# Kernel tuning notes

Measured on AMD Instinct MI355X. Metric: run time of the kernel, lower is better.

## Reference

```python
import jax, jax.numpy as jnp
import numpy as np

D_MODEL = 2048
N_Q_HEADS = 32
N_KV_HEADS = 8
D_HEAD = 64
D_MLP = 8192
NORM_EPS = 1e-5
INIT_RANGE = 0.02
IGNORE = -100000.0
B, S = 2, 2048


def setup_inputs() -> dict:
    key = jax.random.key(0)
    ks = jax.random.split(key, 8)
    return {
        "resid_pre": jax.random.normal(ks[0], (B, S, D_MODEL), dtype=jnp.float32),
        "W_Q": jax.random.normal(ks[1], (N_Q_HEADS, D_MODEL, D_HEAD), dtype=jnp.float32) * INIT_RANGE,
        "W_K": jax.random.normal(ks[2], (N_KV_HEADS, D_MODEL, D_HEAD), dtype=jnp.float32) * INIT_RANGE,
        "W_V": jax.random.normal(ks[3], (N_KV_HEADS, D_MODEL, D_HEAD), dtype=jnp.float32) * INIT_RANGE,
        "W_O": jax.random.normal(ks[4], (N_KV_HEADS, D_HEAD, D_MODEL), dtype=jnp.float32) * INIT_RANGE,
        "g1": jnp.ones((D_MODEL,), jnp.float32),
        "b1": jnp.zeros((D_MODEL,), jnp.float32),
        "g2": jnp.ones((D_MODEL,), jnp.float32),
        "b2": jnp.zeros((D_MODEL,), jnp.float32),
        "W_in": jax.random.normal(ks[5], (D_MODEL, D_MLP), dtype=jnp.float32) * INIT_RANGE,
        "b_in": jnp.zeros((D_MLP,), jnp.float32),
        "W_out": jax.random.normal(ks[6], (D_MLP, D_MODEL), dtype=jnp.float32) * INIT_RANGE,
        "b_out": jnp.zeros((D_MODEL,), jnp.float32),
    }


def rmsnorm(x, g, b):
    # torch.var (unbiased=False) is mean-centered variance, but x itself is
    # divided (not centered) -- faithful to the source.
    mu = jnp.mean(x, axis=-1, keepdims=True)
    var = jnp.mean(jnp.square(x - mu), axis=-1, keepdims=True)
    std = jnp.sqrt(var + NORM_EPS)
    return (x / std) * g + b


def attention(x, W_Q, W_K, W_V, W_O):
    b, s, _ = x.shape
    q = jnp.einsum('bpd,hde->bphe', x, W_Q)            # [b, s, n_q, d_head]
    k = jnp.einsum('bpd,hde->bphe', x, W_K)            # [b, s, n_kv, d_head]
    v = jnp.einsum('bpd,hde->bphe', x, W_V)            # [b, s, n_kv, d_head]
    g_size = N_Q_HEADS // N_KV_HEADS
    # rearrange '(n_kv g) d' with n_kv outer, group inner
    q = q.reshape(b, s, N_KV_HEADS, g_size, D_HEAD)
    # source einsum sums over the group dim (g not in output) -- faithful
    scores = jnp.einsum('bqkgd,bskd->bkqs', q, k) / jnp.sqrt(jnp.float32(D_HEAD))
    mask = jnp.triu(jnp.ones((s, s), dtype=bool), k=1)
    scores = jnp.where(mask, jnp.float32(IGNORE), scores)
    pattern = jax.nn.softmax(scores, axis=-1)          # [b, n_kv, q, s]
    z = jnp.einsum('bskd,bkqs->bqkd', v, pattern)      # [b, q, n_kv, d_head]
    return jnp.einsum('bqkd,kde->bqe', z, W_O)


def ffn(x, W_in, b_in, W_out, b_out):
    pre = jnp.einsum('bpd,dm->bpm', x, W_in) + b_in
    post = jax.nn.relu(pre)
    return jnp.einsum('bpm,md->bpd', post, W_out) + b_out


def reference(resid_pre, W_Q, W_K, W_V, W_O, g1, b1, g2, b2, W_in, b_in, W_out, b_out):
    resid_mid = attention(rmsnorm(resid_pre, g1, b1), W_Q, W_K, W_V, W_O) + resid_pre
    resid_post = ffn(rmsnorm(resid_mid, g2, b2), W_in, b_in, W_out, b_out) + resid_mid
    return resid_post
```

## Files before the change

### kernel.cpp

```cpp
#include <hip/hip_runtime.h>
#include <hip/hip_bf16.h>


using bf16 = __hip_bfloat16;
typedef __bf16 bf16x8_t __attribute__((ext_vector_type(8)));
typedef float  f32x4_t  __attribute__((ext_vector_type(4)));

#define D_MODEL 2048
#define SEQ     2048
#define NB      2
#define NTOK    4096
#define NKV     8
#define DHEAD   64
#define DMLP    8192
#define NQKV    1536

__device__ inline void storev(float* p, float v) { *p = v; }
__device__ inline void storev(bf16* p, float v)  { *p = __float2bfloat16(v); }

__device__ inline __bf16 tobf(float x) {
    union { __hip_bfloat16 h; __bf16 b; } u;
    u.h = __float2bfloat16(x);
    return u.b;
}

__global__ __launch_bounds__(256) void transpose_f32_bf16_kernel(
    const float* __restrict__ in, bf16* __restrict__ out, int K, int N)
{
    __shared__ float tile[32][33];
    const int n0 = blockIdx.x * 32, k0 = blockIdx.y * 32;
    const int tx = threadIdx.x & 31, ty = threadIdx.x >> 5;
    #pragma unroll
    for (int i = 0; i < 32; i += 8)
        tile[ty + i][tx] = in[(size_t)(k0 + ty + i) * N + n0 + tx];
    __syncthreads();
    #pragma unroll
    for (int i = 0; i < 32; i += 8)
        out[(size_t)(n0 + ty + i) * K + k0 + tx] = __float2bfloat16(tile[tx][ty + i]);
}

__global__ __launch_bounds__(256) void head_transpose_kernel(
    const float* __restrict__ in, bf16* __restrict__ out, int ngroup)
{
    __shared__ float tile[32][65];
    const int kv = blockIdx.y;
    const int k0 = blockIdx.x * 32;
    const int t  = threadIdx.x;
    const int e  = t & 63, kk = t >> 6;
    #pragma unroll
    for (int i = 0; i < 32; i += 4) {
        float s = 0.f;
        for (int g = 0; g < ngroup; ++g)
            s += in[((size_t)(kv * ngroup + g) * 2048 + k0 + kk + i) * 64 + e];
        tile[kk + i][e] = s;
    }
    __syncthreads();
    const int k = t & 31, ee = t >> 5;
    #pragma unroll
    for (int i = 0; i < 64; i += 8)
        out[(size_t)(kv * 64 + ee + i) * 2048 + k0 + k] = __float2bfloat16(tile[k][ee + i]);
}

__global__ __launch_bounds__(256) void rmsnorm_kernel(
    const float* __restrict__ x, const float* __restrict__ g,
    const float* __restrict__ b, bf16* __restrict__ out)
{
    const int row = blockIdx.x;
    const int t = threadIdx.x;
    const float* xr = x + (size_t)row * D_MODEL;
    float4 a0 = *reinterpret_cast<const float4*>(xr + t * 8);
    float4 a1 = *reinterpret_cast<const float4*>(xr + t * 8 + 4);
    float v[8] = {a0.x, a0.y, a0.z, a0.w, a1.x, a1.y, a1.z, a1.w};
    float sum = 0.f, sumsq = 0.f;
    #pragma unroll
    for (int j = 0; j < 8; ++j) { sum += v[j]; sumsq += v[j] * v[j]; }
    #pragma unroll
    for (int o = 1; o < 64; o <<= 1) {
        sum   += __shfl_xor(sum, o);
        sumsq += __shfl_xor(sumsq, o);
    }
    __shared__ float rs[4], rq[4];
    if ((t & 63) == 0) { rs[t >> 6] = sum; rq[t >> 6] = sumsq; }
    __syncthreads();
    sum   = rs[0] + rs[1] + rs[2] + rs[3];
    sumsq = rq[0] + rq[1] + rq[2] + rq[3];
    const float mu  = sum * (1.f / D_MODEL);
    const float var = sumsq * (1.f / D_MODEL) - mu * mu;
    const float rstd = 1.f / sqrtf(var + 1e-5f);
    const int c = t * 8;
    float4 g0 = *reinterpret_cast<const float4*>(g + c);
    float4 g1 = *reinterpret_cast<const float4*>(g + c + 4);
    float4 b0 = *reinterpret_cast<const float4*>(b + c);
    float4 b1 = *reinterpret_cast<const float4*>(b + c + 4);
    float gg[8] = {g0.x, g0.y, g0.z, g0.w, g1.x, g1.y, g1.z, g1.w};
    float bb[8] = {b0.x, b0.y, b0.z, b0.w, b1.x, b1.y, b1.z, b1.w};
    bf16* op = out + (size_t)row * D_MODEL + c;
    #pragma unroll
    for (int j = 0; j < 8; ++j) op[j] = __float2bfloat16(v[j] * rstd * gg[j] + bb[j]);
}

template<int BM, typename TC, bool BIAS, bool RELU, bool RESID>
__global__ __launch_bounds__(512, 2) void gemm_pipe_kernel(
    const bf16* __restrict__ A, const bf16* __restrict__ Bt,
    TC* __restrict__ C, const float* __restrict__ bias,
    const float* __restrict__ resid, int M, int N, int K, int nbx)
{
    constexpr int BN   = 256;
    constexpr int BK   = 64;
    constexpr int MREP = BM / 32;
    constexpr int AI   = (BM * BK) / 4096;

    __shared__ __align__(16) bf16 As[2][BM * BK];
    __shared__ __align__(16) bf16 Bs[2][BN * BK];

    const int nwg = gridDim.x;
    const int swz = (blockIdx.x & 7) * (nwg >> 3) + (blockIdx.x >> 3);
    const int nby = nwg / nbx;
    const int by  = swz % nby;
    const int bx  = swz / nby;
    const int row0 = by * BM, col0 = bx * BN;

    const int t  = threadIdx.x;
    const int w  = t >> 6, ln = t & 63;
    const int wm = w >> 2, wn = w & 3;
    const int lr = ln & 15, hi = ln >> 4;

    const int srow = w * 8 + (ln >> 3);
    const int skx  = ((ln & 7) ^ (ln >> 3)) * 8;

    f32x4_t acc[MREP][4];
    #pragma unroll
    for (int m = 0; m < MREP; ++m)
        #pragma unroll
        for (int n = 0; n < 4; ++n) acc[m][n] = (f32x4_t){0.f, 0.f, 0.f, 0.f};

    const int NT = K / BK;

    {
        const bf16* ga = A  + (size_t)(row0 + srow) * K + skx;
        const bf16* gb = Bt + (size_t)(col0 + srow) * K + skx;
        #pragma unroll
        for (int i = 0; i < AI; ++i)
            __builtin_amdgcn_global_load_lds(
                (const __attribute__((address_space(1))) void*)(ga + (size_t)i * 64 * K),
                (__attribute__((address_space(3))) void*)(&As[0][i * 4096 + w * 512]), 16, 0, 0);
        #pragma unroll
        for (int i = 0; i < 4; ++i)
            __builtin_amdgcn_global_load_lds(
                (const __attribute__((address_space(1))) void*)(gb + (size_t)i * 64 * K),
                (__attribute__((address_space(3))) void*)(&Bs[0][i * 4096 + w * 512]), 16, 0, 0);
    }

    for (int tt = 0; tt < NT; ++tt) {
        const int c = tt & 1;
        asm volatile("s_waitcnt lgkmcnt(0)" ::: "memory");
        __builtin_amdgcn_sched_barrier(0);
        __builtin_amdgcn_s_barrier();
        __builtin_amdgcn_sched_barrier(0);
        if (tt + 1 < NT) {
            const int d = c ^ 1;
            const int kt = (tt + 1) * BK;
            const bf16* ga = A  + (size_t)(row0 + srow) * K + kt + skx;
            const bf16* gb = Bt + (size_t)(col0 + srow) * K + kt + skx;
            #pragma unroll
            for (int i = 0; i < AI; ++i)
                __builtin_amdgcn_global_load_lds(
                    (const __attribute__((address_space(1))) void*)(ga + (size_t)i * 64 * K),
                    (__attribute__((address_space(3))) void*)(&As[d][i * 4096 + w * 512]), 16, 0, 0);
            #pragma unroll
            for (int i = 0; i < 4; ++i)
                __builtin_amdgcn_global_load_lds(
                    (const __attribute__((address_space(1))) void*)(gb + (size_t)i * 64 * K),
                    (__attribute__((address_space(3))) void*)(&Bs[d][i * 4096 + w * 512]), 16, 0, 0);
            __builtin_amdgcn_sched_barrier(0);
            if constexpr (AI == 4) asm volatile("s_waitcnt vmcnt(8)" ::: "memory");
            else                   asm volatile("s_waitcnt vmcnt(6)" ::: "memory");
        } else {
            asm volatile("s_waitcnt vmcnt(0)" ::: "memory");
        }
        __builtin_amdgcn_sched_barrier(0);
        __builtin_amdgcn_s_barrier();
        __builtin_amdgcn_sched_barrier(0);

        #pragma unroll
        for (int kk = 0; kk < 2; ++kk) {
            bf16x8_t af[MREP], bfr[4];
            #pragma unroll
            for (int m = 0; m < MREP; ++m) {
                const int row = wm * (BM / 2) + m * 16 + lr;
                af[m] = *reinterpret_cast<const bf16x8_t*>(
                    &As[c][row * 64 + ((kk * 32 + hi * 8) ^ ((row & 7) << 3))]);
            }
            #pragma unroll
            for (int n = 0; n < 4; ++n) {
                const int col = wn * 64 + n * 16 + lr;
                bfr[n] = *reinterpret_cast<const bf16x8_t*>(
                    &Bs[c][col * 64 + ((kk * 32 + hi * 8) ^ ((col & 7) << 3))]);
            }
            #pragma unroll
            for (int m = 0; m < MREP; ++m)
                #pragma unroll
                for (int n = 0; n < 4; ++n)
                    acc[m][n] = __builtin_amdgcn_mfma_f32_16x16x32_bf16(af[m], bfr[n], acc[m][n], 0, 0, 0);
        }
    }

    #pragma unroll
    for (int m = 0; m < MREP; ++m) {
        #pragma unroll
        for (int n = 0; n < 4; ++n) {
            const int cgl = col0 + wn * 64 + n * 16 + lr;
            #pragma unroll
            for (int j = 0; j < 4; ++j) {
                const int r = row0 + wm * (BM / 2) + m * 16 + hi * 4 + j;
                float v = acc[m][n][j];
                if constexpr (BIAS)  v += bias[cgl];
                if constexpr (RELU)  v = fmaxf(v, 0.f);
                if constexpr (RESID) v += resid[(size_t)r * N + cgl];
                storev(&C[(size_t)r * N + cgl], v);
            }
        }
    }
}

#define QBLK  128
#define KVBLK 64
#define LP    72

__global__ __launch_bounds__(512) void mfma_attn_kernel(
    const float* __restrict__ qkv, bf16* __restrict__ z)
{
    const int qt = blockIdx.x;
    const int kv = blockIdx.y;
    const int b  = blockIdx.z;
    const int t  = threadIdx.x;
    const int w  = t >> 6;
    const int ln = t & 63;
    const int lr = ln & 15;
    const int hi = ln >> 4;
    const int lk = hi * 8;

    __shared__ __align__(16) bf16 Ks[KVBLK * LP];
    __shared__ __align__(16) bf16 Vt[DHEAD * LP];
    __shared__ __align__(16) bf16 Ps[QBLK * LP];

    bf16x8_t qf[2];
    {
        const int qrow = qt * QBLK + w * 16 + lr;
        const float* qp = qkv + (size_t)(b * SEQ + qrow) * NQKV + kv * 64;
        #pragma unroll
        for (int kk = 0; kk < 2; ++kk) {
            float4 x0 = *reinterpret_cast<const float4*>(qp + kk * 32 + lk);
            float4 x1 = *reinterpret_cast<const float4*>(qp + kk * 32 + lk + 4);
            bf16x8_t v;
            v[0] = tobf(x0.x); v[1] = tobf(x0.y); v[2] = tobf(x0.z); v[3] = tobf(x0.w);
            v[4] = tobf(x1.x); v[5] = tobf(x1.y); v[6] = tobf(x1.z); v[7] = tobf(x1.w);
            qf[kk] = v;
        }
    }

    f32x4_t acc_o[4];
    #pragma unroll
    for (int n = 0; n < 4; ++n) acc_o[n] = (f32x4_t){0.f, 0.f, 0.f, 0.f};
    float m_st[4] = {-1e30f, -1e30f, -1e30f, -1e30f};
    float l_st[4] = {0.f, 0.f, 0.f, 0.f};

    const int qbase_cd = qt * QBLK + w * 16 + hi * 4;

    const int n_tiles = 2 * qt + 2;
    for (int kt = 0; kt < n_tiles; ++kt) {
        const int k0g = kt * KVBLK;
        __syncthreads();
        {
            const int r  = t >> 3;
            const int c8 = (t & 7) * 8;
            const float* kb = qkv + (size_t)(b * SEQ + k0g + r) * NQKV + 512 + kv * 64 + c8;
            float4 k0 = *reinterpret_cast<const float4*>(kb);
            float4 k1 = *reinterpret_cast<const float4*>(kb + 4);
            bf16x8_t kvv;
            kvv[0] = tobf(k0.x); kvv[1] = tobf(k0.y); kvv[2] = tobf(k0.z); kvv[3] = tobf(k0.w);
            kvv[4] = tobf(k1.x); kvv[5] = tobf(k1.y); kvv[6] = tobf(k1.z); kvv[7] = tobf(k1.w);
            *reinterpret_cast<bf16x8_t*>(&Ks[r * LP + c8]) = kvv;
        }
        {
            const int dv = w * 8;
            const float* vb = qkv + (size_t)(b * SEQ + k0g + ln) * NQKV + 1024 + kv * 64 + dv;
            float4 v0 = *reinterpret_cast<const float4*>(vb);
            float4 v1 = *reinterpret_cast<const float4*>(vb + 4);
            float vv[8] = {v0.x, v0.y, v0.z, v0.w, v1.x, v1.y, v1.z, v1.w};
            #pragma unroll
            for (int i = 0; i < 8; ++i)
                Vt[(dv + i) * LP + ln] = __float2bfloat16(vv[i]);
        }
        __syncthreads();

        f32x4_t s[4];
        #pragma unroll
        for (int n = 0; n < 4; ++n) s[n] = (f32x4_t){0.f, 0.f, 0.f, 0.f};
        #pragma unroll
        for (int kk = 0; kk < 2; ++kk) {
            #pragma unroll
            for (int n = 0; n < 4; ++n) {
                bf16x8_t kf = *reinterpret_cast<const bf16x8_t*>(&Ks[(n * 16 + lr) * LP + kk * 32 + lk]);
                s[n] = __builtin_amdgcn_mfma_f32_16x16x32_bf16(qf[kk], kf, s[n], 0, 0, 0);
            }
        }

        const bool need_mask = (kt >= 2 * qt);
        #pragma unroll
        for (int n = 0; n < 4; ++n) {
            const int colg = k0g + n * 16 + lr;
            #pragma unroll
            for (int j = 0; j < 4; ++j) {
                float val = s[n][j] * 0.125f;
                if (need_mask && colg > qbase_cd + j) val = -1e30f;
                s[n][j] = val;
            }
        }

        float alpha[4], mnew[4];
        #pragma unroll
        for (int j = 0; j < 4; ++j) {
            float mx = fmaxf(fmaxf(s[0][j], s[1][j]), fmaxf(s[2][j], s[3][j]));
            mx = fmaxf(mx, __shfl_xor(mx, 1));
            mx = fmaxf(mx, __shfl_xor(mx, 2));
            mx = fmaxf(mx, __shfl_xor(mx, 4));
            mx = fmaxf(mx, __shfl_xor(mx, 8));
            mnew[j]  = fmaxf(m_st[j], mx);
            alpha[j] = __expf(m_st[j] - mnew[j]);
            m_st[j]  = mnew[j];
        }
        float psum[4] = {0.f, 0.f, 0.f, 0.f};
        #pragma unroll
        for (int n = 0; n < 4; ++n) {
            #pragma unroll
            for (int j = 0; j < 4; ++j) {
                float p = __expf(s[n][j] - mnew[j]);
                psum[j] += p;
                Ps[(w * 16 + hi * 4 + j) * LP + n * 16 + lr] = __float2bfloat16(p);
            }
        }
        #pragma unroll
        for (int j = 0; j < 4; ++j) {
            float ps = psum[j];
            ps += __shfl_xor(ps, 1);
            ps += __shfl_xor(ps, 2);
            ps += __shfl_xor(ps, 4);
            ps += __shfl_xor(ps, 8);
            l_st[j] = l_st[j] * alpha[j] + ps;
        }
        #pragma unroll
        for (int n = 0; n < 4; ++n)
            #pragma unroll
            for (int j = 0; j < 4; ++j)
                acc_o[n][j] *= alpha[j];

        #pragma unroll
        for (int kk = 0; kk < 2; ++kk) {
            bf16x8_t pa = *reinterpret_cast<const bf16x8_t*>(&Ps[(w * 16 + lr) * LP + kk * 32 + lk]);
            #pragma unroll
            for (int n = 0; n < 4; ++n) {
                bf16x8_t vf = *reinterpret_cast<const bf16x8_t*>(&Vt[(n * 16 + lr) * LP + kk * 32 + lk]);
                acc_o[n] = __builtin_amdgcn_mfma_f32_16x16x32_bf16(pa, vf, acc_o[n], 0, 0, 0);
            }
        }
    }

    #pragma unroll
    for (int j = 0; j < 4; ++j) {
        const float inv = 1.f / l_st[j];
        const int tok = b * SEQ + qbase_cd + j;
        bf16* zp = z + (size_t)tok * (NKV * DHEAD) + kv * 64;
        #pragma unroll
        for (int n = 0; n < 4; ++n)
            zp[n * 16 + lr] = __float2bfloat16(acc_o[n][j] * inv);
    }
}

extern "C" void kernel_launch(void* const* d_in, const int* in_sizes, int n_in,
                              void* d_out, int out_size, void* d_ws, size_t ws_size,
                              hipStream_t stream)
{
    const float* resid_pre = (const float*)d_in[0];
    const float* W_Q   = (const float*)d_in[1];
    const float* W_K   = (const float*)d_in[2];
    const float* W_V   = (const float*)d_in[3];
    const float* W_O   = (const float*)d_in[4];
    const float* g1    = (const float*)d_in[5];
    const float* b1    = (const float*)d_in[6];
    const float* g2    = (const float*)d_in[7];
    const float* b2    = (const float*)d_in[8];
    const float* W_in  = (const float*)d_in[9];
    const float* b_in  = (const float*)d_in[10];
    const float* W_out = (const float*)d_in[11];
    const float* b_out = (const float*)d_in[12];
    float* out = (float*)d_out;

    char* ws = (char*)d_ws;
    const size_t OFF_WBIG  = 0;
    const size_t OFF_WOT   = OFF_WBIG + (size_t)DMLP * D_MODEL * 2;
    const size_t OFF_X1    = OFF_WOT  + (size_t)D_MODEL * 512 * 2;
    const size_t OFF_RMID  = OFF_X1   + (size_t)NTOK * D_MODEL * 2;
    const size_t OFF_POST  = OFF_RMID + (size_t)NTOK * D_MODEL * 4;
    const size_t OFF_WQKVT = OFF_POST;
    const size_t OFF_QKV   = OFF_WQKVT + (size_t)NQKV * D_MODEL * 2;
    const size_t OFF_Z     = OFF_QKV   + (size_t)NTOK * NQKV * 4;

    bf16*  winT   = (bf16*) (ws + OFF_WBIG);
    bf16*  woutT  = (bf16*) (ws + OFF_WBIG);
    bf16*  woT    = (bf16*) (ws + OFF_WOT);
    bf16*  x1     = (bf16*) (ws + OFF_X1);
    float* rmid   = (float*)(ws + OFF_RMID);
    bf16*  post   = (bf16*) (ws + OFF_POST);
    bf16*  wqkvT  = (bf16*) (ws + OFF_WQKVT);
    float* qkv    = (float*)(ws + OFF_QKV);
    bf16*  zbuf   = (bf16*) (ws + OFF_Z);

    transpose_f32_bf16_kernel<<<dim3(DMLP / 32, D_MODEL / 32), 256, 0, stream>>>(W_in, winT, D_MODEL, DMLP);
    head_transpose_kernel<<<dim3(D_MODEL / 32, NKV), 256, 0, stream>>>(W_Q, wqkvT, 4);
    head_transpose_kernel<<<dim3(D_MODEL / 32, NKV), 256, 0, stream>>>(W_K, wqkvT + (size_t)512  * D_MODEL, 1);
    head_transpose_kernel<<<dim3(D_MODEL / 32, NKV), 256, 0, stream>>>(W_V, wqkvT + (size_t)1024 * D_MODEL, 1);
    transpose_f32_bf16_kernel<<<dim3(D_MODEL / 32, 512 / 32), 256, 0, stream>>>(W_O, woT, 512, D_MODEL);

    rmsnorm_kernel<<<NTOK, 256, 0, stream>>>(resid_pre, g1, b1, x1);
    gemm_pipe_kernel<128, float, false, false, false><<<192, 512, 0, stream>>>(
        x1, wqkvT, qkv, nullptr, nullptr, NTOK, NQKV, D_MODEL, NQKV / 256);
    mfma_attn_kernel<<<dim3(SEQ / QBLK, NKV, NB), 512, 0, stream>>>(qkv, zbuf);
    gemm_pipe_kernel<128, float, false, false, true><<<256, 512, 0, stream>>>(
        zbuf, woT, rmid, nullptr, resid_pre, NTOK, D_MODEL, 512, D_MODEL / 256);
    rmsnorm_kernel<<<NTOK, 256, 0, stream>>>(rmid, g2, b2, x1);
    gemm_pipe_kernel<256, bf16, true, true, false><<<512, 512, 0, stream>>>(
        x1, winT, post, b_in, nullptr, NTOK, DMLP, D_MODEL, DMLP / 256);
    transpose_f32_bf16_kernel<<<dim3(D_MODEL / 32, DMLP / 32), 256, 0, stream>>>(W_out, woutT, DMLP, D_MODEL);
    gemm_pipe_kernel<128, float, true, false, true><<<256, 512, 0, stream>>>(
        post, woutT, out, b_out, rmid, NTOK, D_MODEL, DMLP, D_MODEL / 256);
}
```

Baseline: 561.3 us.

## Add 8-phase pipelined 256x256 GEMM kernel for FFN up-projection

```diff
diff --git a/kernel.cpp b/kernel.cpp
--- a/kernel.cpp
+++ b/kernel.cpp
@@ -221,6 +221,186 @@
             }
         }
     }
+}
+
+template<typename TC, bool BIAS, bool RELU, bool RESID>
+__global__ __launch_bounds__(512, 2) void gemm_8ph_kernel(
+    const bf16* __restrict__ A, const bf16* __restrict__ Bt,
+    TC* __restrict__ C, const float* __restrict__ bias,
+    const float* __restrict__ resid, int M, int N, int K, int nbx)
+{
+    __shared__ __align__(16) bf16 As[2][256 * 64];
+    __shared__ __align__(16) bf16 Bs[2][256 * 64];
+
+    const int nwg = gridDim.x;
+    const int swz = (blockIdx.x & 7) * (nwg >> 3) + (blockIdx.x >> 3);
+    const int nby = nwg / nbx;
+    const int by  = swz % nby;
+    const int bx  = swz / nby;
+    const int row0 = by * 256, col0 = bx * 256;
+
+    const int t  = threadIdx.x;
+    const int w  = t >> 6, ln = t & 63;
+    const int wm = w >> 2, wn = w & 3;
+    const int lr = ln & 15, hi = ln >> 4;
+    const int rx = (lr & 7) << 3;
+
+    const int srow = w * 8 + (ln >> 3);
+    const int skx  = ((ln & 7) ^ (ln >> 3)) * 8;
+
+#define STAGE_A8(u, dbuf, kt)                                                   \
+    __builtin_amdgcn_global_load_lds(                                           \
+        (const __attribute__((address_space(1))) void*)(A + (size_t)(row0 + (u) * 64 + srow) * K + (kt) + skx), \
+        (__attribute__((address_space(3))) void*)(&As[dbuf][(u) * 4096 + w * 512]), 16, 0, 0)
+#define STAGE_B8(u, dbuf, kt)                                                   \
+    __builtin_amdgcn_global_load_lds(                                           \
+        (const __attribute__((address_space(1))) void*)(Bt + (size_t)(col0 + (u) * 64 + srow) * K + (kt) + skx), \
+        (__attribute__((address_space(3))) void*)(&Bs[dbuf][(u) * 4096 + w * 512]), 16, 0, 0)
+#define PH_BAR                                                                  \
+    __builtin_amdgcn_sched_barrier(0);                                          \
+    __builtin_amdgcn_s_barrier();                                               \
+    __builtin_amdgcn_sched_barrier(0)
+#define LGKM0                                                                   \
+    asm volatile("s_waitcnt lgkmcnt(0)" ::: "memory");                          \
+    __builtin_amdgcn_sched_barrier(0)
+
+    f32x4_t acc[8][4];
+    #pragma unroll
+    for (int m = 0; m < 8; ++m)
+        #pragma unroll
+        for (int n = 0; n < 4; ++n) acc[m][n] = (f32x4_t){0.f, 0.f, 0.f, 0.f};
+
+    bf16x8_t af[4][2];
+    bf16x8_t bfr[4][2];
+
+    const int NT = K / 64;
+
+    STAGE_A8(0, 0, 0); STAGE_A8(2, 0, 0);
+    STAGE_B8(0, 0, 0); STAGE_B8(1, 0, 0); STAGE_B8(2, 0, 0); STAGE_B8(3, 0, 0);
+    STAGE_A8(1, 0, 0); STAGE_A8(3, 0, 0);
+    asm volatile("s_waitcnt vmcnt(2)" ::: "memory");
+    PH_BAR;
+
+    for (int tt = 0; tt < NT; ++tt) {
+        const int c  = tt & 1, d = c ^ 1;
+        const int kn = (tt + 1) * 64;
+        const bool pf = (tt + 1 < NT);
+
+        #pragma unroll
+        for (int mq = 0; mq < 4; ++mq) {
+            const int row = wm * 128 + mq * 16 + lr;
+            #pragma unroll
+            for (int kk = 0; kk < 2; ++kk)
+                af[mq][kk] = *reinterpret_cast<const bf16x8_t*>(
+                    &As[c][row * 64 + ((kk * 32 + hi * 8) ^ rx)]);
+        }
+        #pragma unroll
+        for (int n = 0; n < 2; ++n) {
+            const int col = wn * 64 + n * 16 + lr;
+            #pragma unroll
+            for (int kk = 0; kk < 2; ++kk)
+                bfr[n][kk] = *reinterpret_cast<const bf16x8_t*>(
+                    &Bs[c][col * 64 + ((kk * 32 + hi * 8) ^ rx)]);
+        }
+        if (pf) { STAGE_A8(0, d, kn); STAGE_A8(2, d, kn); }
+        PH_BAR;
+        LGKM0;
+        __builtin_amdgcn_s_setprio(1);
+        #pragma unroll
+        for (int mq = 0; mq < 4; ++mq)
+            #pragma unroll
+            for (int n = 0; n < 2; ++n)
+                #pragma unroll
+                for (int kk = 0; kk < 2; ++kk)
+                    acc[mq][n] = __builtin_amdgcn_mfma_f32_16x16x32_bf16(af[mq][kk], bfr[n][kk], acc[mq][n], 0, 0, 0);
+        __builtin_amdgcn_s_setprio(0);
+        PH_BAR;
+
+        #pragma unroll
+        for (int n = 2; n < 4; ++n) {
+            const int col = wn * 64 + n * 16 + lr;
+            #pragma unroll
+            for (int kk = 0; kk < 2; ++kk)
+                bfr[n][kk] = *reinterpret_cast<const bf16x8_t*>(
+                    &Bs[c][col * 64 + ((kk * 32 + hi * 8) ^ rx)]);
+        }
+        if (pf) { STAGE_B8(0, d, kn); STAGE_B8(1, d, kn); }
+        __builtin_amdgcn_sched_barrier(0);
+        if (pf) { asm volatile("s_waitcnt vmcnt(4)" ::: "memory"); }
+        else    { asm volatile("s_waitcnt vmcnt(0)" ::: "memory"); }
+        PH_BAR;
+        LGKM0;
+        __builtin_amdgcn_s_setprio(1);
+        #pragma unroll
+        for (int mq = 0; mq < 4; ++mq)
+            #pragma unroll
+            for (int n = 2; n < 4; ++n)
+                #pragma unroll
+                for (int kk = 0; kk < 2; ++kk)
+                    acc[mq][n] = __builtin_amdgcn_mfma_f32_16x16x32_bf16(af[mq][kk], bfr[n][kk], acc[mq][n], 0, 0, 0);
+        __builtin_amdgcn_s_setprio(0);
+        PH_BAR;
+
+        #pragma unroll
+        for (int mq = 0; mq < 4; ++mq) {
+            const int row = wm * 128 + 64 + mq * 16 + lr;
+            #pragma unroll
+            for (int kk = 0; kk < 2; ++kk)
+                af[mq][kk] = *reinterpret_cast<const bf16x8_t*>(
+                    &As[c][row * 64 + ((kk * 32 + hi * 8) ^ rx)]);
+        }
+        if (pf) { STAGE_B8(2, d, kn); STAGE_B8(3, d, kn); }
+        PH_BAR;
+        LGKM0;
+        __builtin_amdgcn_s_setprio(1);
+        #pragma unroll
+        for (int mq = 0; mq < 4; ++mq)
+            #pragma unroll
+            for (int n = 2; n < 4; ++n)
+                #pragma unroll
+                for (int kk = 0; kk < 2; ++kk)
+                    acc[4 + mq][n] = __builtin_amdgcn_mfma_f32_16x16x32_bf16(af[mq][kk], bfr[n][kk], acc[4 + mq][n], 0, 0, 0);
+        __builtin_amdgcn_s_setprio(0);
+        PH_BAR;
+
+        if (pf) {
+            STAGE_A8(1, d, kn); STAGE_A8(3, d, kn);
+            __builtin_amdgcn_sched_barrier(0);
+            asm volatile("s_waitcnt vmcnt(2)" ::: "memory");
+        }
+        PH_BAR;
+        __builtin_amdgcn_s_setprio(1);
+        #pragma unroll
+        for (int mq = 0; mq < 4; ++mq)
+            #pragma unroll
+            for (int n = 0; n < 2; ++n)
+                #pragma unroll
+                for (int kk = 0; kk < 2; ++kk)
+                    acc[4 + mq][n] = __builtin_amdgcn_mfma_f32_16x16x32_bf16(af[mq][kk], bfr[n][kk], acc[4 + mq][n], 0, 0, 0);
+        __builtin_amdgcn_s_setprio(0);
+        PH_BAR;
+    }
+
+    #pragma unroll
+    for (int m = 0; m < 8; ++m) {
+        #pragma unroll
+        for (int n = 0; n < 4; ++n) {
+            const int cgl = col0 + wn * 64 + n * 16 + lr;
+            #pragma unroll
+            for (int j = 0; j < 4; ++j) {
+                const int r = row0 + wm * 128 + m * 16 + hi * 4 + j;
+                float v = acc[m][n][j];
+                if constexpr (BIAS)  v += bias[cgl];
+                if constexpr (RELU)  v = fmaxf(v, 0.f);
+                if constexpr (RESID) v += resid[(size_t)r * N + cgl];
+                storev(&C[(size_t)r * N + cgl], v);
+            }
+        }
+    }
+#undef STAGE_A8
+#undef STAGE_B8
+#undef PH_BAR
+#undef LGKM0
 }
 
 #define QBLK  128
@@ -429,7 +609,7 @@
     gemm_pipe_kernel<128, float, false, false, true><<<256, 512, 0, stream>>>(
         zbuf, woT, rmid, nullptr, resid_pre, NTOK, D_MODEL, 512, D_MODEL / 256);
     rmsnorm_kernel<<<NTOK, 256, 0, stream>>>(rmid, g2, b2, x1);
-    gemm_pipe_kernel<256, bf16, true, true, false><<<512, 512, 0, stream>>>(
+    gemm_8ph_kernel<bf16, true, true, false><<<512, 512, 0, stream>>>(
         x1, winT, post, b_in, nullptr, NTOK, DMLP, D_MODEL, DMLP / 256);
     transpose_f32_bf16_kernel<<<dim3(D_MODEL / 32, DMLP / 32), 256, 0, stream>>>(W_out, woutT, DMLP, D_MODEL);
     gemm_pipe_kernel<128, float, true, false, true><<<256, 512, 0, stream>>>(
```

After: 544.9 us. -2.9%, faster.
